# Kernel optimization log

Measured on AMD Instinct MI355X. Metric: run time of the kernel, lower is better.

## Reference

```python
import jax, jax.numpy as jnp
import numpy as np

IN_SIZE = 512
OUT_SIZE = 256
HIDDEN = 256
LN_EPS = 1e-5


def setup_inputs() -> dict:
    key = jax.random.key(0)
    ks = jax.random.split(key, 9)
    B, S, K = 8, 2048, 16
    net_in = jax.random.normal(ks[0], (B, S, K, IN_SIZE), dtype=jnp.float32)
    embeds = jax.random.normal(ks[1], (B, S, OUT_SIZE), dtype=jnp.float32)
    m = jax.random.uniform(ks[2], (B, S, K, 1), dtype=jnp.float32)
    W1 = jax.random.normal(ks[3], (IN_SIZE, HIDDEN), dtype=jnp.float32) * 0.02
    b1 = jnp.full((HIDDEN,), 0.02, dtype=jnp.float32)
    Wf = jax.random.normal(ks[4], (HIDDEN, OUT_SIZE + 1), dtype=jnp.float32) * 0.02
    bf = jnp.zeros((OUT_SIZE + 1,), dtype=jnp.float32)
    gamma = jnp.ones((OUT_SIZE,), dtype=jnp.float32)
    beta = jnp.zeros((OUT_SIZE,), dtype=jnp.float32)
    return {"net_in": net_in, "embeds": embeds, "m": m, "W1": W1, "b1": b1,
            "Wf": Wf, "bf": bf, "gamma": gamma, "beta": beta}


def reference(net_in, embeds, m, W1, b1, Wf, bf, gamma, beta):
    # MLP: one hidden relu layer, final linear to out_size+1
    h = jax.nn.relu(jnp.einsum('bski,ih->bskh', net_in, W1) + b1)
    out = jnp.einsum('bskh,ho->bsko', h, Wf) + bf          # [B,S,K,out+1]
    # sigmoid on last channel (link weight), then mask
    out = jnp.concatenate([out[..., :-1], jax.nn.sigmoid(out[..., -1:])], axis=-1)
    out = m * out
    link_weight = out[..., -1] + 1e-8                       # [B,S,K]
    norm = jnp.sum(link_weight, axis=2, keepdims=True)      # [B,S,1]
    weights = (link_weight / norm)[..., None]               # [B,S,K,1]
    updates = jnp.sum(out * weights, axis=2)                # [B,S,out+1]
    # residual update
    upd_weights = updates[..., -1:]
    embeds_new = embeds + upd_weights * updates[..., :-1]
    # LayerNorm over last dim
    mu = jnp.mean(embeds_new, axis=-1, keepdims=True)
    var = jnp.var(embeds_new, axis=-1, keepdims=True)
    return (embeds_new - mu) * jax.lax.rsqrt(var + LN_EPS) * gamma + beta
```

## Files before the change

### kernel.cpp

```cpp
#include <hip/hip_runtime.h>

typedef short s16x8 __attribute__((ext_vector_type(8)));
typedef float f32x4 __attribute__((ext_vector_type(4)));

__device__ __forceinline__ unsigned short f2bf(float f) {
    union { float f; unsigned u; } v; v.f = f;
    return (unsigned short)((v.u + 0x7FFFu + ((v.u >> 16) & 1u)) >> 16);
}
__device__ __forceinline__ float bf2f(unsigned short h) {
    union { unsigned u; float f; } v; v.u = ((unsigned)h) << 16;
    return v.f;
}

typedef unsigned int u32;
typedef const u32 __attribute__((address_space(1))) gu32;
typedef u32 __attribute__((address_space(3))) lu32;

__device__ __forceinline__ void gload16(const void* g, void* l) {
    __builtin_amdgcn_global_load_lds((gu32*)g, (lu32*)l, 16, 0, 0);
}

#define NBLK 2048

__global__ void prep_weights(const float* __restrict__ W1, const float* __restrict__ Wf,
                             unsigned short* __restrict__ W1T, unsigned short* __restrict__ WfT) {
    int t = blockIdx.x * 256 + threadIdx.x;
    {
        int c  = t >> 13;
        int n  = (t >> 5) & 255;
        int kk = t & 31;
        W1T[t] = f2bf(W1[(c * 32 + kk) * 256 + n]);
    }
    if (t < 65536) {
        int c  = t >> 13;
        int n  = (t >> 5) & 255;
        int hh = t & 31;
        WfT[t] = f2bf(Wf[(c * 32 + hh) * 257 + n]);
    }
}

__global__ __launch_bounds__(512, 2)
void fused_embed(const float* __restrict__ net_in, const float* __restrict__ embeds,
                 const float* __restrict__ mg, const float* __restrict__ W1,
                 const float* __restrict__ b1, const float* __restrict__ Wf,
                 const float* __restrict__ bfv, const float* __restrict__ gam,
                 const float* __restrict__ bet, float* __restrict__ out,
                 const unsigned short* __restrict__ W1T, const unsigned short* __restrict__ WfT)
{
    __shared__ float Abuf[4][128][32];
    __shared__ unsigned short Hbuf[128][260];
    __shared__ unsigned short gbuf[16][264];
    __shared__ float updb[8][264];
    __shared__ float sbuf[8];

    const int tid  = threadIdx.x;
    const int lane = tid & 63;
    const int wid  = tid >> 6;
    const int wr   = wid >> 2;
    const int wc   = wid & 3;
    const int l15  = lane & 15;
    const int g8   = (lane >> 4) * 8;
    const int blk  = blockIdx.x;
    const int row0 = blk * 128;

    const f32x4 zero4 = {0.f, 0.f, 0.f, 0.f};

    f32x4 acc[4][4];
    #pragma unroll
    for (int i = 0; i < 4; ++i)
        #pragma unroll
        for (int j = 0; j < 4; ++j)
            acc[i][j] = zero4;

    const int wbase = (wc * 64 + l15) * 32 + g8;

    const int r0 = tid >> 3, c0 = tid & 7;
    const int r1 = 64 + (tid >> 3);
    const int sc0 = (c0 ^ (r0 & 7)) * 4;
    const int sc1 = (c0 ^ (r1 & 7)) * 4;
    char* const ldsbase = (char*)&Abuf[0][0][0];

    s16x8 wW[2][4];

#define A_DMA(KC) do { \
        char* _d = ldsbase + ((KC) & 3) * 16384 + tid * 16; \
        gload16(net_in + (size_t)(row0 + r0) * 512 + (KC) * 32 + sc0, _d); \
        gload16(net_in + (size_t)(row0 + r1) * 512 + (KC) * 32 + sc1, _d + 8192); \
    } while (0)

#define W_ISSUE(KC, S) do { \
        const unsigned short* _wp = W1T + (KC) * 8192 + wbase; \
        wW[S][0] = *(const s16x8*)(_wp); \
        wW[S][1] = *(const s16x8*)(_wp + 512); \
        wW[S][2] = *(const s16x8*)(_wp + 1024); \
        wW[S][3] = *(const s16x8*)(_wp + 1536); \
    } while (0)

    W_ISSUE(0, 0);
    W_ISSUE(1, 1);
    A_DMA(0); A_DMA(1); A_DMA(2);
    __builtin_amdgcn_sched_barrier(0);
    asm volatile("s_waitcnt vmcnt(4)" ::: "memory");
    __builtin_amdgcn_s_barrier();
    __builtin_amdgcn_sched_barrier(0);

    #pragma unroll
    for (int kc = 0; kc < 16; ++kc) {
        const int slot = kc & 3;
        s16x8 b0 = wW[kc & 1][0], b1r = wW[kc & 1][1], b2 = wW[kc & 1][2], b3 = wW[kc & 1][3];
        if (kc < 14) W_ISSUE(kc + 2, kc & 1);
        if (kc < 13) A_DMA(kc + 3);
        #pragma unroll
        for (int i = 0; i < 4; ++i) {
            const int row = (wr * 4 + i) * 16 + l15;
            const int gx = (lane >> 4) * 2;
            f32x4 lo = *(const f32x4*)&Abuf[slot][row][((gx + 0) ^ (l15 & 7)) * 4];
            f32x4 hi = *(const f32x4*)&Abuf[slot][row][((gx + 1) ^ (l15 & 7)) * 4];
            int4 pk;
            asm("v_cvt_pk_bf16_f32 %0, %1, %2" : "=v"(pk.x) : "v"(lo.x), "v"(lo.y));
            asm("v_cvt_pk_bf16_f32 %0, %1, %2" : "=v"(pk.y) : "v"(lo.z), "v"(lo.w));
            asm("v_cvt_pk_bf16_f32 %0, %1, %2" : "=v"(pk.z) : "v"(hi.x), "v"(hi.y));
            asm("v_cvt_pk_bf16_f32 %0, %1, %2" : "=v"(pk.w) : "v"(hi.z), "v"(hi.w));
            s16x8 af = *(const s16x8*)&pk;
            acc[i][0] = __builtin_amdgcn_mfma_f32_16x16x32_bf16(af, b0, acc[i][0], 0, 0, 0);
            acc[i][1] = __builtin_amdgcn_mfma_f32_16x16x32_bf16(af, b1r, acc[i][1], 0, 0, 0);
            acc[i][2] = __builtin_amdgcn_mfma_f32_16x16x32_bf16(af, b2, acc[i][2], 0, 0, 0);
            acc[i][3] = __builtin_amdgcn_mfma_f32_16x16x32_bf16(af, b3, acc[i][3], 0, 0, 0);
        }
        if (kc < 15) {
            __builtin_amdgcn_sched_barrier(0);
            if (kc == 0)       asm volatile("s_waitcnt vmcnt(8)"  ::: "memory");
            else if (kc <= 12) asm volatile("s_waitcnt vmcnt(12)" ::: "memory");
            else if (kc == 13) asm volatile("s_waitcnt vmcnt(10)" ::: "memory");
            else               asm volatile("s_waitcnt vmcnt(4)"  ::: "memory");
            __builtin_amdgcn_s_barrier();
            __builtin_amdgcn_sched_barrier(0);
        }
    }
#undef A_DMA
#undef W_ISSUE

    #pragma unroll
    for (int j = 0; j < 4; ++j) {
        int col = wc * 64 + j * 16 + l15;
        float bb = b1[col];
        #pragma unroll
        for (int i = 0; i < 4; ++i) {
            #pragma unroll
            for (int r = 0; r < 4; ++r) {
                int row = (wr * 4 + i) * 16 + (lane >> 4) * 4 + r;
                Hbuf[row][col] = f2bf(fmaxf(acc[i][j][r] + bb, 0.f));
            }
        }
    }
    __syncthreads();

    float wl0 = Wf[(lane * 4 + 0) * 257 + 256];
    float wl1 = Wf[(lane * 4 + 1) * 257 + 256];
    float wl2 = Wf[(lane * 4 + 2) * 257 + 256];
    float wl3 = Wf[(lane * 4 + 3) * 257 + 256];
    float bf256 = bfv[256];

    float lcreg = 0.f;
    for (int k = 0; k < 16; ++k) {
        ushort4 hv = *(const ushort4*)&Hbuf[wid * 16 + k][lane * 4];
        float p = bf2f(hv.x) * wl0 + bf2f(hv.y) * wl1 + bf2f(hv.z) * wl2 + bf2f(hv.w) * wl3;
        #pragma unroll
        for (int off = 32; off > 0; off >>= 1) p += __shfl_xor(p, off, 64);
        if (lane == k) lcreg = p;
    }

    float wwreg = 0.f;
    float u256 = 0.f;
    if (lane < 16) {
        float mv  = mg[(blk * 8 + wid) * 16 + lane];
        float raw = lcreg + bf256;
        float sg  = 1.f / (1.f + expf(-raw));
        float v   = mv * sg;
        float lw  = v + 1e-8f;
        float nrm = lw;
        #pragma unroll
        for (int off = 8; off > 0; off >>= 1) nrm += __shfl_xor(nrm, off, 16);
        float wk = lw / nrm;
        wwreg = wk * mv;
        float u = wk * v;
        float s = wwreg;
        #pragma unroll
        for (int off = 8; off > 0; off >>= 1) {
            u += __shfl_xor(u, off, 16);
            s += __shfl_xor(s, off, 16);
        }
        u256 = u;
        if (lane == 0) sbuf[wid] = s;
    }
    u256 = __shfl(u256, 0, 64);

    {
        float ga0 = 0.f, ga1 = 0.f, ga2 = 0.f, ga3 = 0.f;
        #pragma unroll
        for (int k = 0; k < 16; ++k) {
            float wwk = __shfl(wwreg, k, 64);
            ushort4 hv = *(const ushort4*)&Hbuf[wid * 16 + k][lane * 4];
            ga0 += wwk * bf2f(hv.x);
            ga1 += wwk * bf2f(hv.y);
            ga2 += wwk * bf2f(hv.z);
            ga3 += wwk * bf2f(hv.w);
        }
        ushort4 gw; gw.x = f2bf(ga0); gw.y = f2bf(ga1); gw.z = f2bf(ga2); gw.w = f2bf(ga3);
        *(ushort4*)&gbuf[wid][lane * 4] = gw;
        ushort4 z4; z4.x = 0; z4.y = 0; z4.z = 0; z4.w = 0;
        *(ushort4*)&gbuf[8 + wid][lane * 4] = z4;
    }
    __syncthreads();

    f32x4 acc2[2];
    acc2[0] = zero4; acc2[1] = zero4;
    {
        const int w2n0 = ((wid * 2 + 0) * 16 + l15) * 32 + g8;
        const int w2n1 = ((wid * 2 + 1) * 16 + l15) * 32 + g8;
        s16x8 w2a[2], w2b[2];
        w2a[0] = *(const s16x8*)(WfT + w2n0);
        w2b[0] = *(const s16x8*)(WfT + w2n1);
        #pragma unroll
        for (int c2 = 0; c2 < 8; ++c2) {
            const int cur = c2 & 1;
            s16x8 ba = w2a[cur], bb = w2b[cur];
            if (c2 < 7) {
                w2a[cur ^ 1] = *(const s16x8*)(WfT + (c2 + 1) * 8192 + w2n0);
                w2b[cur ^ 1] = *(const s16x8*)(WfT + (c2 + 1) * 8192 + w2n1);
            }
            s16x8 ga = *(const s16x8*)&gbuf[l15][c2 * 32 + g8];
            acc2[0] = __builtin_amdgcn_mfma_f32_16x16x32_bf16(ga, ba, acc2[0], 0, 0, 0);
            acc2[1] = __builtin_amdgcn_mfma_f32_16x16x32_bf16(ga, bb, acc2[1], 0, 0, 0);
        }
    }

    {
        int gq = lane >> 4;
        if (gq < 2) {
            #pragma unroll
            for (int t = 0; t < 2; ++t) {
                int col = (wid * 2 + t) * 16 + l15;
                float bfc = bfv[col];
                #pragma unroll
                for (int r = 0; r < 4; ++r) {
                    int p = gq * 4 + r;
                    updb[p][col] = acc2[t][r] + sbuf[p] * bfc;
                }
            }
        }
    }
    __syncthreads();

    {
        int base = (blk * 8 + wid) * 256;
        float4 up = *(const float4*)&updb[wid][lane * 4];
        float4 em = *(const float4*)&embeds[base + lane * 4];
        float e0 = em.x + u256 * up.x;
        float e1 = em.y + u256 * up.y;
        float e2 = em.z + u256 * up.z;
        float e3 = em.w + u256 * up.w;
        float s1 = e0 + e1 + e2 + e3;
        float s2 = e0 * e0 + e1 * e1 + e2 * e2 + e3 * e3;
        #pragma unroll
        for (int off = 32; off > 0; off >>= 1) {
            s1 += __shfl_xor(s1, off, 64);
            s2 += __shfl_xor(s2, off, 64);
        }
        float mu  = s1 * (1.f / 256.f);
        float var = s2 * (1.f / 256.f) - mu * mu;
        float rs  = rsqrtf(var + 1e-5f);
        float4 gm = *(const float4*)&gam[lane * 4];
        float4 bt = *(const float4*)&bet[lane * 4];
        float4 o;
        o.x = (e0 - mu) * rs * gm.x + bt.x;
        o.y = (e1 - mu) * rs * gm.y + bt.y;
        o.z = (e2 - mu) * rs * gm.z + bt.z;
        o.w = (e3 - mu) * rs * gm.w + bt.w;
        *(float4*)&out[base + lane * 4] = o;
    }
}

extern "C" void kernel_launch(void* const* d_in, const int* in_sizes, int n_in,
                              void* d_out, int out_size, void* d_ws, size_t ws_size,
                              hipStream_t stream) {
    (void)in_sizes; (void)n_in; (void)ws_size; (void)out_size;
    const float* net_in = (const float*)d_in[0];
    const float* embeds = (const float*)d_in[1];
    const float* mg     = (const float*)d_in[2];
    const float* W1     = (const float*)d_in[3];
    const float* b1     = (const float*)d_in[4];
    const float* Wf     = (const float*)d_in[5];
    const float* bfv    = (const float*)d_in[6];
    const float* gam    = (const float*)d_in[7];
    const float* bet    = (const float*)d_in[8];
    float* outp = (float*)d_out;

    unsigned short* W1T = (unsigned short*)d_ws;
    unsigned short* WfT = W1T + 131072;

    prep_weights<<<512, 256, 0, stream>>>(W1, Wf, W1T, WfT);
    fused_embed<<<NBLK, 512, 0, stream>>>(net_in, embeds, mg, W1, b1, Wf, bfv, gam, bet, outp, W1T, WfT);
}
```

Measured before the change: 209.7 us.

## Stage W1 tiles through LDS via async DMA instead of per-wave register loads

```diff
diff --git a/kernel.cpp b/kernel.cpp
--- a/kernel.cpp
+++ b/kernel.cpp
@@ -47,11 +47,20 @@
                  const float* __restrict__ bet, float* __restrict__ out,
                  const unsigned short* __restrict__ W1T, const unsigned short* __restrict__ WfT)
 {
-    __shared__ float Abuf[4][128][32];
-    __shared__ unsigned short Hbuf[128][260];
+    __shared__ union {
+        struct {
+            float Abuf[4][128][32];
+            unsigned short Wbuf[4][256][32];
+        } g1;
+        unsigned short Hbuf[128][260];
+    } U;
     __shared__ unsigned short gbuf[16][264];
     __shared__ float updb[8][264];
     __shared__ float sbuf[8];
+
+    auto& Abuf = U.g1.Abuf;
+    auto& Wbuf = U.g1.Wbuf;
+    auto& Hbuf = U.Hbuf;
 
     const int tid  = threadIdx.x;
     const int lane = tid & 63;
@@ -72,44 +81,46 @@
         for (int j = 0; j < 4; ++j)
             acc[i][j] = zero4;
 
-    const int wbase = (wc * 64 + l15) * 32 + g8;
-
     const int r0 = tid >> 3, c0 = tid & 7;
     const int r1 = 64 + (tid >> 3);
     const int sc0 = (c0 ^ (r0 & 7)) * 4;
     const int sc1 = (c0 ^ (r1 & 7)) * 4;
-    char* const ldsbase = (char*)&Abuf[0][0][0];
-
-    s16x8 wW[2][4];
+    char* const albase = (char*)&Abuf[0][0][0];
+    char* const wlbase = (char*)&Wbuf[0][0][0];
 
 #define A_DMA(KC) do { \
-        char* _d = ldsbase + ((KC) & 3) * 16384 + tid * 16; \
+        char* _d = albase + ((KC) & 3) * 16384 + tid * 16; \
         gload16(net_in + (size_t)(row0 + r0) * 512 + (KC) * 32 + sc0, _d); \
         gload16(net_in + (size_t)(row0 + r1) * 512 + (KC) * 32 + sc1, _d + 8192); \
     } while (0)
 
-#define W_ISSUE(KC, S) do { \
-        const unsigned short* _wp = W1T + (KC) * 8192 + wbase; \
-        wW[S][0] = *(const s16x8*)(_wp); \
-        wW[S][1] = *(const s16x8*)(_wp + 512); \
-        wW[S][2] = *(const s16x8*)(_wp + 1024); \
-        wW[S][3] = *(const s16x8*)(_wp + 1536); \
+#define W_DMA(KC) do { \
+        char* _d = wlbase + ((KC) & 3) * 16384 + tid * 16; \
+        gload16(W1T + (KC) * 8192 + tid * 8, _d); \
+        gload16(W1T + (KC) * 8192 + 4096 + tid * 8, _d + 8192); \
     } while (0)
 
-    W_ISSUE(0, 0);
-    W_ISSUE(1, 1);
-    A_DMA(0); A_DMA(1); A_DMA(2);
+    W_DMA(0); A_DMA(0);
     __builtin_amdgcn_sched_barrier(0);
-    asm volatile("s_waitcnt vmcnt(4)" ::: "memory");
+    W_DMA(1); A_DMA(1);
+    __builtin_amdgcn_sched_barrier(0);
+    W_DMA(2); A_DMA(2);
+    __builtin_amdgcn_sched_barrier(0);
+    asm volatile("s_waitcnt vmcnt(8)" ::: "memory");
     __builtin_amdgcn_s_barrier();
     __builtin_amdgcn_sched_barrier(0);
 
     #pragma unroll
     for (int kc = 0; kc < 16; ++kc) {
         const int slot = kc & 3;
-        s16x8 b0 = wW[kc & 1][0], b1r = wW[kc & 1][1], b2 = wW[kc & 1][2], b3 = wW[kc & 1][3];
-        if (kc < 14) W_ISSUE(kc + 2, kc & 1);
-        if (kc < 13) A_DMA(kc + 3);
+        if (kc < 13) {
+            W_DMA(kc + 3); A_DMA(kc + 3);
+            __builtin_amdgcn_sched_barrier(0);
+        }
+        s16x8 bfrag[4];
+        #pragma unroll
+        for (int j = 0; j < 4; ++j)
+            bfrag[j] = *(const s16x8*)&Wbuf[slot][wc * 64 + j * 16 + l15][g8];
         #pragma unroll
         for (int i = 0; i < 4; ++i) {
             const int row = (wr * 4 + i) * 16 + l15;
@@ -122,23 +133,24 @@
             asm("v_cvt_pk_bf16_f32 %0, %1, %2" : "=v"(pk.z) : "v"(hi.x), "v"(hi.y));
             asm("v_cvt_pk_bf16_f32 %0, %1, %2" : "=v"(pk.w) : "v"(hi.z), "v"(hi.w));
             s16x8 af = *(const s16x8*)&pk;
-            acc[i][0] = __builtin_amdgcn_mfma_f32_16x16x32_bf16(af, b0, acc[i][0], 0, 0, 0);
-            acc[i][1] = __builtin_amdgcn_mfma_f32_16x16x32_bf16(af, b1r, acc[i][1], 0, 0, 0);
-            acc[i][2] = __builtin_amdgcn_mfma_f32_16x16x32_bf16(af, b2, acc[i][2], 0, 0, 0);
-            acc[i][3] = __builtin_amdgcn_mfma_f32_16x16x32_bf16(af, b3, acc[i][3], 0, 0, 0);
+            acc[i][0] = __builtin_amdgcn_mfma_f32_16x16x32_bf16(af, bfrag[0], acc[i][0], 0, 0, 0);
+            acc[i][1] = __builtin_amdgcn_mfma_f32_16x16x32_bf16(af, bfrag[1], acc[i][1], 0, 0, 0);
+            acc[i][2] = __builtin_amdgcn_mfma_f32_16x16x32_bf16(af, bfrag[2], acc[i][2], 0, 0, 0);
+            acc[i][3] = __builtin_amdgcn_mfma_f32_16x16x32_bf16(af, bfrag[3], acc[i][3], 0, 0, 0);
         }
         if (kc < 15) {
             __builtin_amdgcn_sched_barrier(0);
-            if (kc == 0)       asm volatile("s_waitcnt vmcnt(8)"  ::: "memory");
-            else if (kc <= 12) asm volatile("s_waitcnt vmcnt(12)" ::: "memory");
-            else if (kc == 13) asm volatile("s_waitcnt vmcnt(10)" ::: "memory");
-            else               asm volatile("s_waitcnt vmcnt(4)"  ::: "memory");
+            if (kc <= 12)      asm volatile("s_waitcnt vmcnt(8)" ::: "memory");
+            else if (kc == 13) asm volatile("s_waitcnt vmcnt(4)" ::: "memory");
+            else               asm volatile("s_waitcnt vmcnt(0)" ::: "memory");
             __builtin_amdgcn_s_barrier();
             __builtin_amdgcn_sched_barrier(0);
         }
     }
 #undef A_DMA
-#undef W_ISSUE
+#undef W_DMA
+
+    __syncthreads();
 
     #pragma unroll
     for (int j = 0; j < 4; ++j) {
```

Measured after the change: 397.8 us. 89.7% more time.
